# Optimization experiments

Hardware: AMD Instinct MI355X
Metric: run time of the kernel (lower is better)

The kernel has to match this reference:

```python
import jax, jax.numpy as jnp
import numpy as np
from jax import lax

STRIDE = 1
PAD = 1  # module pads 1 on each side whenever padding != 0


def setup_inputs() -> dict:
    key = jax.random.key(0)
    kx, kw, kb = jax.random.split(key, 3)
    x = jax.random.normal(kx, (4096, 4096), dtype=jnp.float32)
    weight = jax.random.normal(kw, (15, 15), dtype=jnp.float32)
    bias = jax.random.normal(kb, (1,), dtype=jnp.float32)
    return {"x": x, "weight": weight, "bias": bias}


def reference(x, weight, bias):
    # Single-channel 2D cross-correlation with constant zero padding of 1 and
    # stride STRIDE, plus a scalar bias. lax.conv_general_dilated computes
    # correlation (no kernel flip), matching the torch corr2d loop exactly.
    out = lax.conv_general_dilated(
        x[None, None, :, :],          # NCHW, N=C=1
        weight[None, None, :, :],      # OIHW, O=I=1
        window_strides=(STRIDE, STRIDE),
        padding=[(PAD, PAD), (PAD, PAD)],
        dimension_numbers=("NCHW", "OIHW", "NCHW"),
    )[0, 0]
    return out + bias[0]
```

## Files before the change

kernel.cpp:

```cpp
#include <hip/hip_runtime.h>

#define IN_N   4096
#define OW     4084
#define KS     15
#define XS     88
#define WROWS  30
#define NBX    64
#define NBY    128

typedef __attribute__((ext_vector_type(8))) short     v8s;
typedef __attribute__((ext_vector_type(8))) _Float16  v8h;
typedef __attribute__((ext_vector_type(4))) float     v4f;
typedef __attribute__((ext_vector_type(2))) float     v2f;
typedef __attribute__((ext_vector_type(4))) unsigned  v4u;

__global__ void build_B(const float* __restrict__ w, unsigned short* __restrict__ Bg) {
    int ky = blockIdx.x;
    int e  = threadIdx.x;
    int n = e & 15, quad = e >> 4;
    unsigned short vals[8];
    #pragma unroll
    for (int j = 0; j < 8; ++j) {
        int d = quad * 8 + j - 1 - n;
        _Float16 h = (_Float16)0.0f;
        if (d >= 0 && d < KS) h = (_Float16)w[ky * KS + d];
        union { _Float16 hh; unsigned short u; } cv; cv.hh = h;
        vals[j] = cv.u;
    }
    *(v8s*)(&Bg[(ky * 64 + e) * 8]) = *(const v8s*)vals;
}

__device__ __forceinline__ unsigned pk(float a, float b) {
    return __builtin_bit_cast(unsigned, __builtin_amdgcn_cvt_pkrtz(a, b));
}

__global__ __launch_bounds__(128, 7) void conv2d_mfma4(
    const float* __restrict__ x, const unsigned short* __restrict__ Bg,
    const float* __restrict__ bias, float* __restrict__ out)
{
    __shared__ unsigned short xtile[2 * WROWS * XS] __attribute__((aligned(16)));

    const int tid  = threadIdx.x;
    const int lane = tid & 63;
    const int wv   = tid >> 6;
    const int bx   = blockIdx.x;
    const int RT   = blockIdx.y * 2 + wv;
    const int X0   = bx * 64;
    const int R0   = RT * 16;

    unsigned short* slice = &xtile[wv * (WROWS * XS)];

    const bool interior = (bx >= 1) & (bx <= 62) & (RT >= 1) & (RT <= 254);

    if (lane < 60) {
        const int r0 = lane / 10;
        const int cu = lane % 10;
        unsigned short* dst = slice + r0 * XS + cu * 8;
        if (interior) {
            const float* xr = x + (size_t)(R0 - 1 + r0) * IN_N + (X0 - 2 + cu * 8);
            #pragma unroll
            for (int i = 0; i < 5; ++i) {
                v2f f0 = *(const v2f*)(xr + 0);
                v2f f1 = *(const v2f*)(xr + 2);
                v2f f2 = *(const v2f*)(xr + 4);
                v2f f3 = *(const v2f*)(xr + 6);
                v4u p;
                p.x = pk(f0.x, f0.y);
                p.y = pk(f1.x, f1.y);
                p.z = pk(f2.x, f2.y);
                p.w = pk(f3.x, f3.y);
                *(v4u*)dst = p;
                xr  += 6 * (size_t)IN_N;
                dst += 6 * XS;
            }
        } else {
            const int gc0 = X0 - 2 + cu * 8;
            #pragma unroll
            for (int i = 0; i < 5; ++i) {
                const int r  = r0 + 6 * i;
                const int gr = R0 - 1 + r;
                float f[8];
                #pragma unroll
                for (int j = 0; j < 8; ++j) f[j] = 0.0f;
                if ((unsigned)gr < (unsigned)IN_N) {
                    const float* xr = x + (size_t)gr * IN_N;
                    #pragma unroll
                    for (int j = 0; j < 8; ++j)
                        if ((unsigned)(gc0 + j) < (unsigned)IN_N) f[j] = xr[gc0 + j];
                }
                v4u p;
                p.x = pk(f[0], f[1]);
                p.y = pk(f[2], f[3]);
                p.z = pk(f[4], f[5]);
                p.w = pk(f[6], f[7]);
                *(v4u*)(slice + r * XS + cu * 8) = p;
            }
        }
    }

    asm volatile("s_waitcnt lgkmcnt(0)" ::: "memory");
    __builtin_amdgcn_sched_barrier(0);

    const int m    = lane & 15;
    const int quad = lane >> 4;

    v4f acc[4];
    #pragma unroll
    for (int t = 0; t < 4; ++t) acc[t] = (v4f){0.f, 0.f, 0.f, 0.f};

    const v8h* Bgv = (const v8h*)Bg;
    const unsigned short* arow = slice + m * XS + quad * 8;

    v8h bcur = Bgv[lane];
    v8h a0 = *(const v8h*)(arow + 0);
    v8h a1 = *(const v8h*)(arow + 16);
    v8h a2 = *(const v8h*)(arow + 32);
    v8h a3 = *(const v8h*)(arow + 48);

    #pragma unroll
    for (int ky = 0; ky < KS; ++ky) {
        const unsigned short* nrow = arow + XS;
        v8h bn = bcur, n0 = a0, n1 = a1, n2 = a2, n3 = a3;
        if (ky < KS - 1) {
            bn = Bgv[(ky + 1) * 64 + lane];
            n0 = *(const v8h*)(nrow + 0);
            n1 = *(const v8h*)(nrow + 16);
            n2 = *(const v8h*)(nrow + 32);
            n3 = *(const v8h*)(nrow + 48);
        }
        acc[0] = __builtin_amdgcn_mfma_f32_16x16x32_f16(a0, bcur, acc[0], 0, 0, 0);
        acc[1] = __builtin_amdgcn_mfma_f32_16x16x32_f16(a1, bcur, acc[1], 0, 0, 0);
        acc[2] = __builtin_amdgcn_mfma_f32_16x16x32_f16(a2, bcur, acc[2], 0, 0, 0);
        acc[3] = __builtin_amdgcn_mfma_f32_16x16x32_f16(a3, bcur, acc[3], 0, 0, 0);
        a0 = n0; a1 = n1; a2 = n2; a3 = n3; bcur = bn;
        arow = nrow;
    }

    const float bv = bias[0];
    const int orow0 = R0 + quad * 4;
    const int ocol0 = X0 + m;
    if ((bx < NBX - 1) & (RT < 255)) {
        float* o0 = &out[(size_t)orow0 * OW + ocol0];
        #pragma unroll
        for (int t = 0; t < 4; ++t) {
            #pragma unroll
            for (int r = 0; r < 4; ++r)
                o0[(size_t)r * OW + t * 16] = acc[t][r] + bv;
        }
    } else {
        #pragma unroll
        for (int t = 0; t < 4; ++t) {
            int oc = ocol0 + t * 16;
            if (oc < OW) {
                #pragma unroll
                for (int r = 0; r < 4; ++r) {
                    int orow = orow0 + r;
                    if (orow < OW)
                        out[(size_t)orow * OW + oc] = acc[t][r] + bv;
                }
            }
        }
    }
}

extern "C" void kernel_launch(void* const* d_in, const int* in_sizes, int n_in,
                              void* d_out, int out_size, void* d_ws, size_t ws_size,
                              hipStream_t stream) {
    const float* x    = (const float*)d_in[0];
    const float* w    = (const float*)d_in[1];
    const float* bias = (const float*)d_in[2];
    float* out        = (float*)d_out;
    unsigned short* Bg = (unsigned short*)d_ws;

    build_B<<<dim3(KS), dim3(64), 0, stream>>>(w, Bg);
    dim3 grid(NBX, NBY);
    conv2d_mfma4<<<grid, dim3(128), 0, stream>>>(x, Bg, bias, out);
}
```

Before: 156.7 us.

## Share halo slab across four waves and double-buffer row tiles per block

Each block now stages a 78-row fp16 slab shared by four waves covering 64 output rows, instead of per-wave 30-row slices. This reduces redundant halo reads from global memory. The block loops over four row tiles, prefetching the next slab into registers before the MFMA loop and writing it to the alternate LDS buffer afterward, to overlap loads with compute. The change adds register pressure and __syncthreads, and uses far fewer blocks, which may lower occupancy and parallel slack.

```diff
diff --git a/kernel.cpp b/kernel.cpp
--- a/kernel.cpp
+++ b/kernel.cpp
@@ -4,9 +4,10 @@
 #define OW     4084
 #define KS     15
 #define XS     88
-#define WROWS  30
+#define XROWS  78
+#define TILES  4
 #define NBX    64
-#define NBY    128
+#define NBY    16
 
 typedef __attribute__((ext_vector_type(8))) short     v8s;
 typedef __attribute__((ext_vector_type(8))) _Float16  v8h;
@@ -34,51 +35,63 @@
     return __builtin_bit_cast(unsigned, __builtin_amdgcn_cvt_pkrtz(a, b));
 }
 
-__global__ __launch_bounds__(128, 7) void conv2d_mfma4(
+__global__ __launch_bounds__(256, 4) void conv2d_mfma5(
     const float* __restrict__ x, const unsigned short* __restrict__ Bg,
     const float* __restrict__ bias, float* __restrict__ out)
 {
-    __shared__ unsigned short xtile[2 * WROWS * XS] __attribute__((aligned(16)));
-
-    const int tid  = threadIdx.x;
+    __shared__ unsigned short xtile[2][XROWS * XS] __attribute__((aligned(16)));
+
+    const int tid = threadIdx.x;
+    const int bx = blockIdx.x, by = blockIdx.y;
+    const int X0  = bx * 64;
+    const int RT0 = by * TILES;
+
+    const int u  = tid % 10;
+    const int r0 = tid / 10;
+    const bool stager = (tid < 240);
+    const bool colInt = (bx >= 1) & (bx <= 62);
+
     const int lane = tid & 63;
     const int wv   = tid >> 6;
-    const int bx   = blockIdx.x;
-    const int RT   = blockIdx.y * 2 + wv;
-    const int X0   = bx * 64;
-    const int R0   = RT * 16;
-
-    unsigned short* slice = &xtile[wv * (WROWS * XS)];
-
-    const bool interior = (bx >= 1) & (bx <= 62) & (RT >= 1) & (RT <= 254);
-
-    if (lane < 60) {
-        const int r0 = lane / 10;
-        const int cu = lane % 10;
-        unsigned short* dst = slice + r0 * XS + cu * 8;
-        if (interior) {
-            const float* xr = x + (size_t)(R0 - 1 + r0) * IN_N + (X0 - 2 + cu * 8);
-            #pragma unroll
-            for (int i = 0; i < 5; ++i) {
-                v2f f0 = *(const v2f*)(xr + 0);
-                v2f f1 = *(const v2f*)(xr + 2);
-                v2f f2 = *(const v2f*)(xr + 4);
-                v2f f3 = *(const v2f*)(xr + 6);
+    const int m    = lane & 15;
+    const int quad = lane >> 4;
+    const v8h* Bgv = (const v8h*)Bg;
+    const float bv = bias[0];
+
+    v2f L[4][4];
+
+    auto load_int = [&](int R0) {
+        const float* xp = x + (size_t)(R0 - 1 + r0) * IN_N + (X0 - 2 + 8 * u);
+        #pragma unroll
+        for (int i = 0; i < 4; ++i) {
+            if (i < 3 || r0 < 6) {
+                const float* xr = xp + (size_t)(24 * i) * IN_N;
+                #pragma unroll
+                for (int j = 0; j < 4; ++j) L[i][j] = *(const v2f*)(xr + 2 * j);
+            }
+        }
+    };
+    auto write_int = [&](unsigned short* buf) {
+        #pragma unroll
+        for (int i = 0; i < 4; ++i) {
+            if (i < 3 || r0 < 6) {
                 v4u p;
-                p.x = pk(f0.x, f0.y);
-                p.y = pk(f1.x, f1.y);
-                p.z = pk(f2.x, f2.y);
-                p.w = pk(f3.x, f3.y);
-                *(v4u*)dst = p;
-                xr  += 6 * (size_t)IN_N;
-                dst += 6 * XS;
-            }
-        } else {
-            const int gc0 = X0 - 2 + cu * 8;
-            #pragma unroll
-            for (int i = 0; i < 5; ++i) {
-                const int r  = r0 + 6 * i;
-                const int gr = R0 - 1 + r;
+                p.x = pk(L[i][0].x, L[i][0].y);
+                p.y = pk(L[i][1].x, L[i][1].y);
+                p.z = pk(L[i][2].x, L[i][2].y);
+                p.w = pk(L[i][3].x, L[i][3].y);
+                *(v4u*)(buf + (r0 + 24 * i) * XS + 8 * u) = p;
+            }
+        }
+    };
+    auto stage_edge = [&](unsigned short* buf, int R0) {
+        if (!stager) return;
+        const int gc0 = X0 - 2 + 8 * u;
+        #pragma unroll
+        for (int i = 0; i < 4; ++i) {
+            int r = r0 + 24 * i;
+            if (r < XROWS) {
+                int gr = R0 - 1 + r;
                 float f[8];
                 #pragma unroll
                 for (int j = 0; j < 8; ++j) f[j] = 0.0f;
@@ -89,77 +102,96 @@
                         if ((unsigned)(gc0 + j) < (unsigned)IN_N) f[j] = xr[gc0 + j];
                 }
                 v4u p;
-                p.x = pk(f[0], f[1]);
-                p.y = pk(f[2], f[3]);
-                p.z = pk(f[4], f[5]);
-                p.w = pk(f[6], f[7]);
-                *(v4u*)(slice + r * XS + cu * 8) = p;
-            }
+                p.x = pk(f[0], f[1]); p.y = pk(f[2], f[3]);
+                p.z = pk(f[4], f[5]); p.w = pk(f[6], f[7]);
+                *(v4u*)(buf + r * XS + 8 * u) = p;
+            }
+        }
+    };
+
+    {
+        const int RT = RT0;
+        const bool tint = colInt & (RT >= 1) & (RT <= 62);
+        if (tint) {
+            if (stager) { load_int(RT * 64); write_int(&xtile[0][0]); }
+        } else {
+            stage_edge(&xtile[0][0], RT * 64);
         }
     }
-
-    asm volatile("s_waitcnt lgkmcnt(0)" ::: "memory");
-    __builtin_amdgcn_sched_barrier(0);
-
-    const int m    = lane & 15;
-    const int quad = lane >> 4;
-
-    v4f acc[4];
-    #pragma unroll
-    for (int t = 0; t < 4; ++t) acc[t] = (v4f){0.f, 0.f, 0.f, 0.f};
-
-    const v8h* Bgv = (const v8h*)Bg;
-    const unsigned short* arow = slice + m * XS + quad * 8;
-
-    v8h bcur = Bgv[lane];
-    v8h a0 = *(const v8h*)(arow + 0);
-    v8h a1 = *(const v8h*)(arow + 16);
-    v8h a2 = *(const v8h*)(arow + 32);
-    v8h a3 = *(const v8h*)(arow + 48);
-
-    #pragma unroll
-    for (int ky = 0; ky < KS; ++ky) {
-        const unsigned short* nrow = arow + XS;
-        v8h bn = bcur, n0 = a0, n1 = a1, n2 = a2, n3 = a3;
-        if (ky < KS - 1) {
-            bn = Bgv[(ky + 1) * 64 + lane];
-            n0 = *(const v8h*)(nrow + 0);
-            n1 = *(const v8h*)(nrow + 16);
-            n2 = *(const v8h*)(nrow + 32);
-            n3 = *(const v8h*)(nrow + 48);
-        }
-        acc[0] = __builtin_amdgcn_mfma_f32_16x16x32_f16(a0, bcur, acc[0], 0, 0, 0);
-        acc[1] = __builtin_amdgcn_mfma_f32_16x16x32_f16(a1, bcur, acc[1], 0, 0, 0);
-        acc[2] = __builtin_amdgcn_mfma_f32_16x16x32_f16(a2, bcur, acc[2], 0, 0, 0);
-        acc[3] = __builtin_amdgcn_mfma_f32_16x16x32_f16(a3, bcur, acc[3], 0, 0, 0);
-        a0 = n0; a1 = n1; a2 = n2; a3 = n3; bcur = bn;
-        arow = nrow;
-    }
-
-    const float bv = bias[0];
-    const int orow0 = R0 + quad * 4;
-    const int ocol0 = X0 + m;
-    if ((bx < NBX - 1) & (RT < 255)) {
-        float* o0 = &out[(size_t)orow0 * OW + ocol0];
-        #pragma unroll
-        for (int t = 0; t < 4; ++t) {
+    __syncthreads();
+
+    for (int t = 0; t < TILES; ++t) {
+        const unsigned short* cur = &xtile[t & 1][0];
+        unsigned short* nxt = &xtile[(t + 1) & 1][0];
+        const int RT = RT0 + t;
+        const int R0 = RT * 64;
+        const bool nxtExists = (t + 1 < TILES);
+        const bool nint = colInt & ((RT + 1) <= 62);
+
+        if (nxtExists & nint) { if (stager) load_int((RT + 1) * 64); }
+        __builtin_amdgcn_sched_barrier(0);
+
+        v4f acc[4];
+        #pragma unroll
+        for (int c = 0; c < 4; ++c) acc[c] = (v4f){0.f, 0.f, 0.f, 0.f};
+
+        const unsigned short* arow = cur + (wv * 16 + m) * XS + quad * 8;
+        v8h bcur = Bgv[lane];
+        v8h a0 = *(const v8h*)(arow + 0);
+        v8h a1 = *(const v8h*)(arow + 16);
+        v8h a2 = *(const v8h*)(arow + 32);
+        v8h a3 = *(const v8h*)(arow + 48);
+
+        #pragma unroll
+        for (int ky = 0; ky < KS; ++ky) {
+            const unsigned short* nrow = arow + XS;
+            v8h bn = bcur, n0 = a0, n1 = a1, n2 = a2, n3 = a3;
+            if (ky < KS - 1) {
+                bn = Bgv[(ky + 1) * 64 + lane];
+                n0 = *(const v8h*)(nrow + 0);
+                n1 = *(const v8h*)(nrow + 16);
+                n2 = *(const v8h*)(nrow + 32);
+                n3 = *(const v8h*)(nrow + 48);
+            }
+            acc[0] = __builtin_amdgcn_mfma_f32_16x16x32_f16(a0, bcur, acc[0], 0, 0, 0);
+            acc[1] = __builtin_amdgcn_mfma_f32_16x16x32_f16(a1, bcur, acc[1], 0, 0, 0);
+            acc[2] = __builtin_amdgcn_mfma_f32_16x16x32_f16(a2, bcur, acc[2], 0, 0, 0);
+            acc[3] = __builtin_amdgcn_mfma_f32_16x16x32_f16(a3, bcur, acc[3], 0, 0, 0);
+            a0 = n0; a1 = n1; a2 = n2; a3 = n3; bcur = bn;
+            arow = nrow;
+        }
+
+        const int orow0 = R0 + wv * 16 + quad * 4;
+        const int ocol0 = X0 + m;
+        if ((bx < NBX - 1) & (RT < 63)) {
+            float* o0 = &out[(size_t)orow0 * OW + ocol0];
             #pragma unroll
-            for (int r = 0; r < 4; ++r)
-                o0[(size_t)r * OW + t * 16] = acc[t][r] + bv;
-        }
-    } else {
-        #pragma unroll
-        for (int t = 0; t < 4; ++t) {
-            int oc = ocol0 + t * 16;
-            if (oc < OW) {
+            for (int c = 0; c < 4; ++c) {
                 #pragma unroll
-                for (int r = 0; r < 4; ++r) {
-                    int orow = orow0 + r;
-                    if (orow < OW)
-                        out[(size_t)orow * OW + oc] = acc[t][r] + bv;
+                for (int r = 0; r < 4; ++r)
+                    o0[(size_t)r * OW + c * 16] = acc[c][r] + bv;
+            }
+        } else {
+            #pragma unroll
+            for (int c = 0; c < 4; ++c) {
+                int oc = ocol0 + c * 16;
+                if (oc < OW) {
+                    #pragma unroll
+                    for (int r = 0; r < 4; ++r) {
+                        int orow = orow0 + r;
+                        if (orow < OW)
+                            out[(size_t)orow * OW + oc] = acc[c][r] + bv;
+                    }
                 }
             }
         }
+        __builtin_amdgcn_sched_barrier(0);
+
+        if (nxtExists) {
+            if (nint) { if (stager) write_int(nxt); }
+            else      stage_edge(nxt, (RT + 1) * 64);
+        }
+        __syncthreads();
     }
 }
 
@@ -174,5 +206,5 @@
 
     build_B<<<dim3(KS), dim3(64), 0, stream>>>(w, Bg);
     dim3 grid(NBX, NBY);
-    conv2d_mfma4<<<grid, dim3(128), 0, stream>>>(x, Bg, bias, out);
-}
+    conv2d_mfma5<<<grid, dim3(256), 0, stream>>>(x, Bg, bias, out);
+}
```

Result: slower. 190.0 us (+21.2%).

## Share one wide LDS input tile across four waves per block

Applied to the files above, without the earlier changes.

Each block now covers 256 output columns by 16 rows with four waves. The waves share a single 30x272 half-precision LDS tile, where before each wave staged its own 64-column slice. This cuts the redundant halo loads of overlapping input columns and the global read traffic per output. The cost is a block-wide __syncthreads in place of per-wave waitcnt, a larger LDS footprint per block, and fewer, larger blocks.

```diff
diff --git a/kernel.cpp b/kernel.cpp
--- a/kernel.cpp
+++ b/kernel.cpp
@@ -3,10 +3,11 @@
 #define IN_N   4096
 #define OW     4084
 #define KS     15
-#define XS     88
-#define WROWS  30
-#define NBX    64
-#define NBY    128
+#define XS     280
+#define XROWS  30
+#define XCOLS  272
+#define NCG    16
+#define NRT    256
 
 typedef __attribute__((ext_vector_type(8))) short     v8s;
 typedef __attribute__((ext_vector_type(8))) _Float16  v8h;
@@ -34,32 +35,28 @@
     return __builtin_bit_cast(unsigned, __builtin_amdgcn_cvt_pkrtz(a, b));
 }
 
-__global__ __launch_bounds__(128, 7) void conv2d_mfma4(
+__global__ __launch_bounds__(256, 8) void conv2d_mfma6(
     const float* __restrict__ x, const unsigned short* __restrict__ Bg,
     const float* __restrict__ bias, float* __restrict__ out)
 {
-    __shared__ unsigned short xtile[2 * WROWS * XS] __attribute__((aligned(16)));
+    __shared__ unsigned short xtile[XROWS * XS] __attribute__((aligned(16)));
 
-    const int tid  = threadIdx.x;
-    const int lane = tid & 63;
-    const int wv   = tid >> 6;
-    const int bx   = blockIdx.x;
-    const int RT   = blockIdx.y * 2 + wv;
-    const int X0   = bx * 64;
-    const int R0   = RT * 16;
+    const int tid = threadIdx.x;
+    const int cg = blockIdx.x;
+    const int rt = blockIdx.y;
+    const int X0 = cg * 256;
+    const int R0 = rt * 16;
 
-    unsigned short* slice = &xtile[wv * (WROWS * XS)];
+    const bool interior = (cg >= 1) & (cg <= 14) & (rt >= 1) & (rt <= 254);
 
-    const bool interior = (bx >= 1) & (bx <= 62) & (RT >= 1) & (RT <= 254);
-
-    if (lane < 60) {
-        const int r0 = lane / 10;
-        const int cu = lane % 10;
-        unsigned short* dst = slice + r0 * XS + cu * 8;
-        if (interior) {
-            const float* xr = x + (size_t)(R0 - 1 + r0) * IN_N + (X0 - 2 + cu * 8);
-            #pragma unroll
-            for (int i = 0; i < 5; ++i) {
+    if (interior) {
+        #pragma unroll
+        for (int s = 0; s < 4; ++s) {
+            int i = s * 256 + tid;
+            if (i < XROWS * 34) {
+                int row = i / 34;
+                int u   = i - 34 * row;
+                const float* xr = x + (size_t)(R0 - 1 + row) * IN_N + (X0 - 2 + 8 * u);
                 v2f f0 = *(const v2f*)(xr + 0);
                 v2f f1 = *(const v2f*)(xr + 2);
                 v2f f2 = *(const v2f*)(xr + 4);
@@ -69,16 +66,18 @@
                 p.y = pk(f1.x, f1.y);
                 p.z = pk(f2.x, f2.y);
                 p.w = pk(f3.x, f3.y);
-                *(v4u*)dst = p;
-                xr  += 6 * (size_t)IN_N;
-                dst += 6 * XS;
+                *(v4u*)(&xtile[row * XS + 8 * u]) = p;
             }
-        } else {
-            const int gc0 = X0 - 2 + cu * 8;
-            #pragma unroll
-            for (int i = 0; i < 5; ++i) {
-                const int r  = r0 + 6 * i;
-                const int gr = R0 - 1 + r;
+        }
+    } else {
+        #pragma unroll
+        for (int s = 0; s < 4; ++s) {
+            int i = s * 256 + tid;
+            if (i < XROWS * 34) {
+                int row = i / 34;
+                int u   = i - 34 * row;
+                int gr  = R0 - 1 + row;
+                int gc0 = X0 - 2 + 8 * u;
                 float f[8];
                 #pragma unroll
                 for (int j = 0; j < 8; ++j) f[j] = 0.0f;
@@ -89,18 +88,16 @@
                         if ((unsigned)(gc0 + j) < (unsigned)IN_N) f[j] = xr[gc0 + j];
                 }
                 v4u p;
-                p.x = pk(f[0], f[1]);
-                p.y = pk(f[2], f[3]);
-                p.z = pk(f[4], f[5]);
-                p.w = pk(f[6], f[7]);
-                *(v4u*)(slice + r * XS + cu * 8) = p;
+                p.x = pk(f[0], f[1]); p.y = pk(f[2], f[3]);
+                p.z = pk(f[4], f[5]); p.w = pk(f[6], f[7]);
+                *(v4u*)(&xtile[row * XS + 8 * u]) = p;
             }
         }
     }
+    __syncthreads();
 
-    asm volatile("s_waitcnt lgkmcnt(0)" ::: "memory");
-    __builtin_amdgcn_sched_barrier(0);
-
+    const int lane = tid & 63;
+    const int wv   = tid >> 6;
     const int m    = lane & 15;
     const int quad = lane >> 4;
 
@@ -109,7 +106,7 @@
     for (int t = 0; t < 4; ++t) acc[t] = (v4f){0.f, 0.f, 0.f, 0.f};
 
     const v8h* Bgv = (const v8h*)Bg;
-    const unsigned short* arow = slice + m * XS + quad * 8;
+    const unsigned short* arow = &xtile[m * XS + 64 * wv + quad * 8];
 
     v8h bcur = Bgv[lane];
     v8h a0 = *(const v8h*)(arow + 0);
@@ -138,8 +135,8 @@
 
     const float bv = bias[0];
     const int orow0 = R0 + quad * 4;
-    const int ocol0 = X0 + m;
-    if ((bx < NBX - 1) & (RT < 255)) {
+    const int ocol0 = X0 + 64 * wv + m;
+    if ((ocol0 + 48 < OW) & (R0 + 15 < OW)) {
         float* o0 = &out[(size_t)orow0 * OW + ocol0];
         #pragma unroll
         for (int t = 0; t < 4; ++t) {
@@ -173,6 +170,6 @@
     unsigned short* Bg = (unsigned short*)d_ws;
 
     build_B<<<dim3(KS), dim3(64), 0, stream>>>(w, Bg);
-    dim3 grid(NBX, NBY);
-    conv2d_mfma4<<<grid, dim3(128), 0, stream>>>(x, Bg, bias, out);
+    dim3 grid(NCG, NRT);
+    conv2d_mfma6<<<grid, dim3(256), 0, stream>>>(x, Bg, bias, out);
 }
```

Result: slower. 166.6 us (+6.3%).
